# Kernel tuning notes

Measured on AMD Instinct MI355X. Metric: run time of the kernel, lower is better.

Reference implementation:

```python
import jax, jax.numpy as jnp
import numpy as np

D_MODEL = 768
N_HEAD = 12


def setup_inputs() -> dict:
    key = jax.random.key(0)
    k1, k2, k3, k4, k5 = jax.random.split(key, 5)
    B, T, C = 4, 2048, D_MODEL
    s = 1.0 / np.sqrt(C)
    return {
        "x": jax.random.normal(k1, (B, T, C), dtype=jnp.float32),
        "w_attn": jax.random.normal(k2, (C, 3 * C), dtype=jnp.float32) * s,
        "b_attn": jax.random.normal(k3, (3 * C,), dtype=jnp.float32) * 0.02,
        "w_proj": jax.random.normal(k4, (C, C), dtype=jnp.float32) * s,
        "b_proj": jax.random.normal(k5, (C,), dtype=jnp.float32) * 0.02,
    }


def reference(x, w_attn, b_attn, w_proj, b_proj):
    B, T, C = x.shape
    H = N_HEAD
    Dh = C // H
    qkv = x @ w_attn + b_attn                      # [B, T, 3C]
    q, k, v = jnp.split(qkv, 3, axis=-1)
    # [B, H, T, Dh]
    q = q.reshape(B, T, H, Dh).transpose(0, 2, 1, 3)
    k = k.reshape(B, T, H, Dh).transpose(0, 2, 1, 3)
    v = v.reshape(B, T, H, Dh).transpose(0, 2, 1, 3)
    att = jnp.einsum("bhqd,bhkd->bhqk", q, k) * (1.0 / np.sqrt(Dh))
    causal = jnp.tril(jnp.ones((T, T), dtype=bool))
    att = jnp.where(causal[None, None, :, :], att, -jnp.inf)
    att = jax.nn.softmax(att, axis=-1)             # dropout p=0 (eval)
    y = jnp.einsum("bhqk,bhkd->bhqd", att, v)      # [B, H, T, Dh]
    y = y.transpose(0, 2, 1, 3).reshape(B, T, C)
    return y @ w_proj + b_proj
```

## Files before the change

kernel.cpp:

```cpp
#include <hip/hip_runtime.h>
#include <stdint.h>

#define NHEAD 12
#define DH 64
#define BATCH 4
#define SEQ 2048
#define CDIM 768
#define MROWS (BATCH*SEQ)

typedef __attribute__((ext_vector_type(8))) short short8;
typedef __attribute__((ext_vector_type(4))) float floatx4;
typedef __attribute__((ext_vector_type(16))) float floatx16;
typedef unsigned int u32;

__device__ inline unsigned short f2bf(float f) {
    union { float f; unsigned u; } v; v.f = f;
    unsigned r = v.u + 0x7FFFu + ((v.u >> 16) & 1u);
    return (unsigned short)(r >> 16);
}

__device__ __forceinline__ u32 pk_bf16(float a, float b) {
    u32 d;
    asm("v_cvt_pk_bf16_f32 %0, %1, %2" : "=v"(d) : "v"(a), "v"(b));
    return d;
}

__device__ __forceinline__ void async_cp16(const unsigned short* g, unsigned short* l) {
    __builtin_amdgcn_global_load_lds(
        (const __attribute__((address_space(1))) u32*)g,
        (__attribute__((address_space(3))) u32*)l, 16, 0, 0);
}

template<int N> __device__ __forceinline__ void waitcnt_vm() {
    if constexpr (N == 0)      asm volatile("s_waitcnt vmcnt(0)" ::: "memory");
    else if constexpr (N == 3) asm volatile("s_waitcnt vmcnt(3)" ::: "memory");
    else if constexpr (N == 4) asm volatile("s_waitcnt vmcnt(4)" ::: "memory");
}

__device__ __forceinline__ void transpose_tile(
    const float* __restrict__ in, unsigned short* __restrict__ out,
    int K, int N, int k0, int n0, unsigned short (*T)[72]) {
    const int t = threadIdx.x;
    const int nc = t & 63, kw = t >> 6;
    for (int i = 0; i < 16; i++) {
        const int kr = kw + i * 4;
        T[nc][kr] = f2bf(in[(size_t)(k0 + kr) * N + n0 + nc]);
    }
    __syncthreads();
    const int row = t >> 2, seg = t & 3;
    uint4 a = *(const uint4*)&T[row][seg * 16];
    uint4 b2 = *(const uint4*)&T[row][seg * 16 + 8];
    unsigned short* o = &out[(size_t)(n0 + row) * K + k0 + seg * 16];
    *(uint4*)o = a;
    *(uint4*)(o + 8) = b2;
}

__global__ __launch_bounds__(256) void prep_kernel(
    const float* __restrict__ x,      unsigned short* __restrict__ xb,
    const float* __restrict__ wa,     unsigned short* __restrict__ wta,
    const float* __restrict__ wp,     unsigned short* __restrict__ wtp) {
    __shared__ unsigned short T[64][72];
    const int lin = blockIdx.x;
    if (lin < 6144) {
        const int i = (lin * 256 + threadIdx.x) * 4;
        float4 f = *(const float4*)(x + i);
        union { unsigned short s[4]; uint2 u; } p;
        p.s[0] = f2bf(f.x); p.s[1] = f2bf(f.y);
        p.s[2] = f2bf(f.z); p.s[3] = f2bf(f.w);
        *(uint2*)(xb + i) = p.u;
    } else if (lin < 6144 + 432) {
        const int t2 = lin - 6144;
        transpose_tile(wa, wta, CDIM, 3 * CDIM, (t2 % 12) * 64, (t2 / 12) * 64, T);
    } else {
        const int t3 = lin - 6576;
        transpose_tile(wp, wtp, CDIM, CDIM, (t3 % 12) * 64, (t3 / 12) * 64, T);
    }
}

template<int MODE, int KD, int BM, int BN>
__global__ __launch_bounds__(256) void gemm_bf16(
    const unsigned short* __restrict__ A,
    const unsigned short* __restrict__ BT,
    const float* __restrict__ bias,
    float* __restrict__ Cout,
    unsigned short* __restrict__ Qout,
    unsigned short* __restrict__ Kout,
    unsigned short* __restrict__ VTout,
    int Ndim)
{
    constexpr int TM = BM / 32, TN = BN / 32;
    constexpr int CHA = BM / 64, CHB = BN / 64;
    __shared__ unsigned short SH[3 * (BM + BN) * 32];
    auto As = [&](int b3) { return &SH[b3 * BM * 32]; };
    auto Bs = [&](int b3) { return &SH[3 * BM * 32 + b3 * BN * 32]; };

    const int tid  = threadIdx.x;
    const int wave = tid >> 6;
    const int lane = tid & 63;
    const int l16  = lane & 15;
    const int quad = lane >> 4;
    const int wm = wave >> 1, wn = wave & 1;
    const int m0 = blockIdx.x * BM;
    const int n0 = blockIdx.y * BN;

    const int rloc = lane >> 2;
    const int gs   = (((lane & 3) ^ (rloc & 3) ^ ((rloc >> 2) & 3))) * 8;
    const int pg   = ((quad ^ (l16 & 3) ^ ((l16 >> 2) & 3))) * 8;

    floatx4 acc[TM][TN];
    for (int i = 0; i < TM; i++)
        for (int j = 0; j < TN; j++) acc[i][j] = (floatx4)0.0f;

    constexpr int NIT = KD / 32;

    auto stageTo = [&](int s, int buf) {
        const int koff = s * 32;
        for (int ch = 0; ch < CHA; ch++) {
            const int row = wave * CHA * 16 + ch * 16 + rloc;
            async_cp16(&A[(size_t)(m0 + row) * KD + koff + gs],
                       &As(buf)[(wave * CHA + ch) * 512]);
        }
        for (int ch = 0; ch < CHB; ch++) {
            const int row = wave * CHB * 16 + ch * 16 + rloc;
            async_cp16(&BT[(size_t)(n0 + row) * KD + koff + gs],
                       &Bs(buf)[(wave * CHB + ch) * 512]);
        }
    };
    stageTo(0, 0);
    stageTo(1, 1);

    int buf = 0;
    for (int it = 0; it < NIT; it++) {
        if (it < NIT - 1) waitcnt_vm<CHA + CHB>();
        else              waitcnt_vm<0>();
        asm volatile("s_barrier" ::: "memory");
        if (it + 2 < NIT) {
            int b2 = buf + 2; if (b2 >= 3) b2 -= 3;
            stageTo(it + 2, b2);
        }
        short8 a[TM], b[TN];
        for (int i = 0; i < TM; i++)
            a[i] = *(const short8*)&As(buf)[(wm * (BM / 2) + i * 16 + l16) * 32 + pg];
        for (int j = 0; j < TN; j++)
            b[j] = *(const short8*)&Bs(buf)[(wn * (BN / 2) + j * 16 + l16) * 32 + pg];
        for (int i = 0; i < TM; i++)
            for (int j = 0; j < TN; j++)
                acc[i][j] = __builtin_amdgcn_mfma_f32_16x16x32_bf16(
                    a[i], b[j], acc[i][j], 0, 0, 0);
        buf++; if (buf >= 3) buf = 0;
    }

    const float QSCALE = 0.18033688011112042f;

    if (MODE == 1 && (n0 / CDIM) == 2) {
        __syncthreads();
        unsigned short* scr = &SH[wave * (64 * 68)];
        for (int i = 0; i < TM; i++) {
            const int tl = i * 16 + quad * 4;
            for (int j = 0; j < TN; j++) {
                const int dl = j * 16 + l16;
                const float bv = bias[n0 + wn * 64 + j * 16 + l16];
                uint2 u;
                u.x = pk_bf16(acc[i][j][0] + bv, acc[i][j][1] + bv);
                u.y = pk_bf16(acc[i][j][2] + bv, acc[i][j][3] + bv);
                *(uint2*)&scr[dl * 68 + tl] = u;
            }
        }
        const int b_ = m0 >> 11;
        const int tg = (m0 & 2047) + wm * 64;
        const int h  = (n0 - 2 * CDIM + wn * 64) >> 6;
        const size_t rowbase = ((size_t)(b_ * NHEAD + h)) * DH;
        for (int p = 0; p < 8; p++) {
            const int d  = p * 8 + (lane >> 3);
            const int tc = (lane & 7) * 8;
            uint4 v = *(const uint4*)&scr[d * 68 + tc];
            *(uint4*)&VTout[(rowbase + d) * SEQ + tg + tc] = v;
        }
        return;
    }

    for (int i = 0; i < TM; i++) {
        const int mbase = m0 + wm * (BM / 2) + i * 16 + quad * 4;
        for (int j = 0; j < TN; j++) {
            const int ncj  = n0 + wn * (BN / 2) + j * 16;
            const int ncol = ncj + l16;
            const float bv = bias[ncol];
            for (int r = 0; r < 4; r++) {
                const int m = mbase + r;
                const float v = acc[i][j][r] + bv;
                if (MODE == 0) {
                    Cout[(size_t)m * Ndim + ncol] = v;
                } else {
                    const int part = ncj / CDIM;
                    const int c = ncol - part * CDIM;
                    const int hh = c >> 6, d = c & 63;
                    const int b_ = m >> 11, t = m & 2047;
                    const size_t bh = (size_t)(b_ * NHEAD + hh);
                    if (part == 0)
                        Qout[(bh * SEQ + t) * DH + d] = f2bf(v * QSCALE);
                    else
                        Kout[(bh * SEQ + t) * DH + d] = f2bf(v);
                }
            }
        }
    }
}

__global__ __launch_bounds__(256) void attn_kernel(
    const unsigned short* __restrict__ Q,
    const unsigned short* __restrict__ K,
    const unsigned short* __restrict__ VT,
    unsigned short* __restrict__ O)
{
    __shared__ unsigned short Kl[3][2][64 * 32];
    __shared__ unsigned short Vl[3][2][64 * 32];

    const int tid  = threadIdx.x;
    const int wave = tid >> 6;
    const int lane = tid & 63;
    const int rl   = lane & 31;
    const int hi   = lane >> 5;
    const int qg   = wave >> 1;
    const int ks   = wave & 1;

    const int lin = blockIdx.x;
    const int grp = lin >> 3;
    const int xs  = grp & 15;
    const int bh  = ((grp >> 4) << 3) | (lin & 7);
    const int h = bh % NHEAD, b = bh / NHEAD;

    const unsigned short* Qp = Q  + (size_t)bh * SEQ * DH;
    const unsigned short* Kp = K  + (size_t)bh * SEQ * DH;
    const unsigned short* Vp = VT + (size_t)bh * DH * SEQ;

    const int rloc  = lane >> 2;
    const int gofsK = ((lane & 3) ^ (rloc & 3) ^ ((rloc >> 2) & 3)) * 8;
    const int krow  = wave * 16 + rloc;
    const int swz   = (rl & 3) ^ ((rl >> 2) & 3);

    for (int pass = 0; pass < 2; pass++) {
        const int qtile = pass == 0 ? xs : 31 - xs;
        const int qb = qtile * 64;
        const int nkt = qtile + 1;

        short8 aq[4];
#pragma unroll
        for (int dc = 0; dc < 4; dc++)
            aq[dc] = *(const short8*)
                &Qp[(size_t)(qb + qg * 32 + rl) * DH + dc * 16 + hi * 8];

        floatx16 accO[2];
        accO[0] = (floatx16)0.0f;
        accO[1] = (floatx16)0.0f;
        float lp = 0.0f;

        auto stage = [&](int kt, int bufb) {
#pragma unroll
            for (int c = 0; c < 2; c++) {
                async_cp16(&Kp[(size_t)(kt * 64 + krow) * DH + c * 32 + gofsK],
                           &Kl[bufb][c][wave * 512]);
                async_cp16(&Vp[(size_t)krow * SEQ + kt * 64 + c * 32 + gofsK],
                           &Vl[bufb][c][wave * 512]);
            }
        };

        stage(0, 0);
        if (nkt > 1) stage(1, 1);

        for (int kt = 0; kt < nkt; kt++) {
            int cur = kt % 3;
            if (kt < nkt - 1) waitcnt_vm<4>();
            else              waitcnt_vm<0>();
            asm volatile("s_barrier" ::: "memory");
            if (kt + 2 < nkt) stage(kt + 2, (kt + 2) % 3);

            const int kq = (kt - qtile) * 64 + (ks - qg) * 32;
            if (kq <= 0) {
                floatx16 s = (floatx16)0.0f;
#pragma unroll
                for (int dc = 0; dc < 4; dc++) {
                    const int p = (((dc & 1) * 2 + hi) ^ swz);
                    const short8 ak = *(const short8*)
                        &Kl[cur][dc >> 1][(ks * 32 + rl) * 32 + p * 8];
                    s = __builtin_amdgcn_mfma_f32_32x32x16_bf16(ak, aq[dc], s, 0, 0, 0);
                }
                if (kq == 0) {
#pragma unroll
                    for (int r = 0; r < 16; r++) {
                        const int kl = (r & 3) + 8 * (r >> 2) + 4 * hi;
                        if (kl > rl) s[r] = -1e30f;
                    }
                }
                float pe[16];
#pragma unroll
                for (int r = 0; r < 16; r++) { pe[r] = exp2f(s[r]); lp += pe[r]; }
                u32 u[8];
#pragma unroll
                for (int i = 0; i < 8; i++) u[i] = pk_bf16(pe[2 * i], pe[2 * i + 1]);

#pragma unroll
                for (int ksl = 0; ksl < 2; ksl++) {
                    union { short8 v; u32 w[4]; } pa;
                    pa.w[0] = u[4 * ksl + 0]; pa.w[1] = u[4 * ksl + 1];
                    pa.w[2] = u[4 * ksl + 2]; pa.w[3] = u[4 * ksl + 3];
                    const int p1 = (2 * ksl) ^ swz;
#pragma unroll
                    for (int db = 0; db < 2; db++) {
                        const int drow = db * 32 + rl;
                        union { short8 v; u32 w[4]; } bv;
                        const uint2 v1 = *(const uint2*)
                            &Vl[cur][ks][drow * 32 + p1 * 8 + hi * 4];
                        const uint2 v2 = *(const uint2*)
                            &Vl[cur][ks][drow * 32 + (p1 ^ 1) * 8 + hi * 4];
                        bv.w[0] = v1.x; bv.w[1] = v1.y; bv.w[2] = v2.x; bv.w[3] = v2.y;
                        accO[db] = __builtin_amdgcn_mfma_f32_32x32x16_bf16(
                            pa.v, bv.v, accO[db], 0, 0, 0);
                    }
                }
            }
        }

        float Lw = lp + __shfl_xor(lp, 32);
        __syncthreads();
        float* redO = (float*)&Kl[0][0][0];
        float* redL = (float*)&Vl[0][0][0];
        if (ks == 1) {
#pragma unroll
            for (int db = 0; db < 2; db++)
#pragma unroll
                for (int r = 0; r < 16; r++)
                    redO[(qg * 32 + db * 16 + r) * 64 + lane] = accO[db][r];
            if (hi == 0) redL[qg * 32 + rl] = Lw;
        }
        __syncthreads();
        if (ks == 0) {
            const float inv = 1.0f / (Lw + redL[qg * 32 + rl]);
#pragma unroll
            for (int r = 0; r < 16; r++) {
                const int qrow = (r & 3) + 8 * (r >> 2) + 4 * hi;
                const float iv = __shfl(inv, qrow, 64);
                const int t = qb + qg * 32 + qrow;
                const size_t base = ((size_t)b * SEQ + t) * CDIM + h * DH;
#pragma unroll
                for (int db = 0; db < 2; db++) {
                    const float o = accO[db][r]
                                  + redO[(qg * 32 + db * 16 + r) * 64 + lane];
                    O[base + db * 32 + rl] = f2bf(o * iv);
                }
            }
        }
        __syncthreads();
    }
}

extern "C" void kernel_launch(void* const* d_in, const int* in_sizes, int n_in,
                              void* d_out, int out_size, void* d_ws, size_t ws_size,
                              hipStream_t stream) {
    const float* x      = (const float*)d_in[0];
    const float* w_attn = (const float*)d_in[1];
    const float* b_attn = (const float*)d_in[2];
    const float* w_proj = (const float*)d_in[3];
    const float* b_proj = (const float*)d_in[4];
    float* out = (float*)d_out;

    unsigned short* xb   = (unsigned short*)d_ws;
    unsigned short* wta  = xb  + (size_t)MROWS * CDIM;
    unsigned short* wtp  = wta + (size_t)3 * CDIM * CDIM;
    unsigned short* qws  = wtp + (size_t)CDIM * CDIM;
    unsigned short* kws  = qws + (size_t)MROWS * CDIM;
    unsigned short* vtws = kws + (size_t)MROWS * CDIM;
    unsigned short* ob   = xb;

    prep_kernel<<<6720, 256, 0, stream>>>(x, xb, w_attn, wta, w_proj, wtp);

    dim3 g1(MROWS / 128, (3 * CDIM) / 128);
    gemm_bf16<1, CDIM, 128, 128><<<g1, 256, 0, stream>>>(
        xb, wta, b_attn, nullptr, qws, kws, vtws, 3 * CDIM);

    attn_kernel<<<768, 256, 0, stream>>>(qws, kws, vtws, ob);

    dim3 g3(MROWS / 64, CDIM / 128);
    gemm_bf16<0, CDIM, 64, 128><<<g3, 256, 0, stream>>>(
        ob, wtp, b_proj, out, nullptr, nullptr, nullptr, CDIM);
}
```

Baseline: 233.7 us.

## Compute softmax row sums via MFMA with ones and unroll ring buffer by three

The softmax denominator is now accumulated by an extra MFMA of the bf16 probabilities against a ones vector, replacing the per-lane scalar adds and the final shuffle. The KV loop is unrolled three ways with compile-time buffer indices so LDS addresses become constants instead of kt%3 arithmetic. exp2f is replaced by the raw hardware exp2 builtin. The trade is an extra MFMA per slice and more code size; the denominator now sums bf16-rounded values, which matches what the PV product uses.

After: 212.3 us. 9.2% less time.

```diff
diff --git a/kernel.cpp b/kernel.cpp
--- a/kernel.cpp
+++ b/kernel.cpp
@@ -12,6 +12,8 @@
 typedef __attribute__((ext_vector_type(4))) float floatx4;
 typedef __attribute__((ext_vector_type(16))) float floatx16;
 typedef unsigned int u32;
+
+template<int N> struct IC { static constexpr int v = N; };
 
 __device__ inline unsigned short f2bf(float f) {
     union { float f; unsigned u; } v; v.f = f;
@@ -238,6 +240,11 @@
     const int krow  = wave * 16 + rloc;
     const int swz   = (rl & 3) ^ ((rl >> 2) & 3);
 
+    union { short8 s; u32 w[4]; } onesU;
+    onesU.w[0] = onesU.w[1] = onesU.w[2] = onesU.w[3] = 0x3F803F80u;
+    const short8 ones = onesU.s;
+    const floatx16 fz = (floatx16)0.0f;
+
     for (int pass = 0; pass < 2; pass++) {
         const int qtile = pass == 0 ? xs : 31 - xs;
         const int qb = qtile * 64;
@@ -250,38 +257,37 @@
                 &Qp[(size_t)(qb + qg * 32 + rl) * DH + dc * 16 + hi * 8];
 
         floatx16 accO[2];
-        accO[0] = (floatx16)0.0f;
-        accO[1] = (floatx16)0.0f;
-        float lp = 0.0f;
-
-        auto stage = [&](int kt, int bufb) {
+        accO[0] = fz; accO[1] = fz;
+        floatx16 accL = fz;
+
+        auto stage = [&](int kt, int tgt) {
 #pragma unroll
             for (int c = 0; c < 2; c++) {
                 async_cp16(&Kp[(size_t)(kt * 64 + krow) * DH + c * 32 + gofsK],
-                           &Kl[bufb][c][wave * 512]);
+                           &Kl[tgt][c][wave * 512]);
                 async_cp16(&Vp[(size_t)krow * SEQ + kt * 64 + c * 32 + gofsK],
-                           &Vl[bufb][c][wave * 512]);
+                           &Vl[tgt][c][wave * 512]);
             }
         };
 
         stage(0, 0);
         if (nkt > 1) stage(1, 1);
 
-        for (int kt = 0; kt < nkt; kt++) {
-            int cur = kt % 3;
+        auto tile = [&](auto CURc, int kt) {
+            constexpr int CUR = decltype(CURc)::v;
             if (kt < nkt - 1) waitcnt_vm<4>();
             else              waitcnt_vm<0>();
             asm volatile("s_barrier" ::: "memory");
-            if (kt + 2 < nkt) stage(kt + 2, (kt + 2) % 3);
+            if (kt + 2 < nkt) stage(kt + 2, (CUR + 2) % 3);
 
             const int kq = (kt - qtile) * 64 + (ks - qg) * 32;
             if (kq <= 0) {
-                floatx16 s = (floatx16)0.0f;
+                floatx16 s = fz;
 #pragma unroll
                 for (int dc = 0; dc < 4; dc++) {
                     const int p = (((dc & 1) * 2 + hi) ^ swz);
                     const short8 ak = *(const short8*)
-                        &Kl[cur][dc >> 1][(ks * 32 + rl) * 32 + p * 8];
+                        &Kl[CUR][dc >> 1][(ks * 32 + rl) * 32 + p * 8];
                     s = __builtin_amdgcn_mfma_f32_32x32x16_bf16(ak, aq[dc], s, 0, 0, 0);
                 }
                 if (kq == 0) {
@@ -291,12 +297,12 @@
                         if (kl > rl) s[r] = -1e30f;
                     }
                 }
-                float pe[16];
-#pragma unroll
-                for (int r = 0; r < 16; r++) { pe[r] = exp2f(s[r]); lp += pe[r]; }
+#pragma unroll
+                for (int r = 0; r < 16; r++) s[r] = __builtin_amdgcn_exp2f(s[r]);
+
                 u32 u[8];
 #pragma unroll
-                for (int i = 0; i < 8; i++) u[i] = pk_bf16(pe[2 * i], pe[2 * i + 1]);
+                for (int i = 0; i < 8; i++) u[i] = pk_bf16(s[2 * i], s[2 * i + 1]);
 
 #pragma unroll
                 for (int ksl = 0; ksl < 2; ksl++) {
@@ -309,44 +315,58 @@
                         const int drow = db * 32 + rl;
                         union { short8 v; u32 w[4]; } bv;
                         const uint2 v1 = *(const uint2*)
-                            &Vl[cur][ks][drow * 32 + p1 * 8 + hi * 4];
+                            &Vl[CUR][ks][drow * 32 + p1 * 8 + hi * 4];
                         const uint2 v2 = *(const uint2*)
-                            &Vl[cur][ks][drow * 32 + (p1 ^ 1) * 8 + hi * 4];
+                            &Vl[CUR][ks][drow * 32 + (p1 ^ 1) * 8 + hi * 4];
                         bv.w[0] = v1.x; bv.w[1] = v1.y; bv.w[2] = v2.x; bv.w[3] = v2.y;
                         accO[db] = __builtin_amdgcn_mfma_f32_32x32x16_bf16(
                             pa.v, bv.v, accO[db], 0, 0, 0);
                     }
+                    accL = __builtin_amdgcn_mfma_f32_32x32x16_bf16(
+                        pa.v, ones, accL, 0, 0, 0);
                 }
             }
-        }
-
-        float Lw = lp + __shfl_xor(lp, 32);
+        };
+
+        int kt = 0;
+        while (kt + 3 <= nkt) {
+            tile(IC<0>{}, kt);
+            tile(IC<1>{}, kt + 1);
+            tile(IC<2>{}, kt + 2);
+            kt += 3;
+        }
+        if (kt < nkt) { tile(IC<0>{}, kt); kt++; }
+        if (kt < nkt) { tile(IC<1>{}, kt); }
+
         __syncthreads();
         float* redO = (float*)&Kl[0][0][0];
         float* redL = (float*)&Vl[0][0][0];
         if (ks == 1) {
 #pragma unroll
-            for (int db = 0; db < 2; db++)
-#pragma unroll
-                for (int r = 0; r < 16; r++)
-                    redO[(qg * 32 + db * 16 + r) * 64 + lane] = accO[db][r];
-            if (hi == 0) redL[qg * 32 + rl] = Lw;
+            for (int r = 0; r < 16; r++) {
+                redO[(qg * 32 + r)      * 64 + lane] = accO[0][r];
+                redO[(qg * 32 + 16 + r) * 64 + lane] = accO[1][r];
+            }
+            if (rl == 0) {
+#pragma unroll
+                for (int r = 0; r < 16; r++) {
+                    const int qrow = (r & 3) + 8 * (r >> 2) + 4 * hi;
+                    redL[qg * 32 + qrow] = accL[r];
+                }
+            }
         }
         __syncthreads();
         if (ks == 0) {
-            const float inv = 1.0f / (Lw + redL[qg * 32 + rl]);
 #pragma unroll
             for (int r = 0; r < 16; r++) {
                 const int qrow = (r & 3) + 8 * (r >> 2) + 4 * hi;
-                const float iv = __shfl(inv, qrow, 64);
+                const float inv = 1.0f / (accL[r] + redL[qg * 32 + qrow]);
                 const int t = qb + qg * 32 + qrow;
                 const size_t base = ((size_t)b * SEQ + t) * CDIM + h * DH;
-#pragma unroll
-                for (int db = 0; db < 2; db++) {
-                    const float o = accO[db][r]
-                                  + redO[(qg * 32 + db * 16 + r) * 64 + lane];
-                    O[base + db * 32 + rl] = f2bf(o * iv);
-                }
+                const float o0 = accO[0][r] + redO[(qg * 32 + r)      * 64 + lane];
+                const float o1 = accO[1][r] + redO[(qg * 32 + 16 + r) * 64 + lane];
+                O[base + rl]      = f2bf(o0 * inv);
+                O[base + 32 + rl] = f2bf(o1 * inv);
             }
         }
         __syncthreads();
```
